# Kernel tuning notes

Hardware: AMD Instinct MI355X
Metric: run time of the kernel (lower is better)

Reference implementation:

```python
import math
import jax, jax.numpy as jnp
import numpy as np
from jax import lax

B = 32768
D = 1024          # input_dim
LAT = 64          # latent_dim
S_SLOTS = 32
L_SLOTS = 256


def setup_inputs() -> dict:
    key = jax.random.key(0)
    ks = jax.random.split(key, 8)
    inp = {
        "query": jax.random.normal(ks[0], (B, D), dtype=jnp.float32),
        "short_term_bank": jax.random.normal(ks[1], (S_SLOTS, D), dtype=jnp.float32) * 0.02,
        "long_term_bank": jax.random.normal(ks[2], (L_SLOTS, LAT), dtype=jnp.float32) * 0.02,
        # long_term_decoder: Linear(LAT -> D), stored as (in, out)
        "dec_w": jax.random.normal(ks[3], (LAT, D), dtype=jnp.float32) / math.sqrt(LAT),
        "dec_b": jnp.zeros((D,), dtype=jnp.float32),
        # query_proj: Linear(D -> LAT)
        "q_w": jax.random.normal(ks[4], (D, LAT), dtype=jnp.float32) / math.sqrt(D),
        "q_b": jnp.zeros((LAT,), dtype=jnp.float32),
        # short_query_proj: Linear(D -> D)
        "sq_w": jax.random.normal(ks[5], (D, D), dtype=jnp.float32) / math.sqrt(D),
        "sq_b": jnp.zeros((D,), dtype=jnp.float32),
        "top_k_short": 4,
        "top_k_long": 8,
    }
    return inp


def reference(query, short_term_bank, long_term_bank, dec_w, dec_b,
              q_w, q_b, sq_w, sq_b, top_k_short, top_k_long):
    # ---- short-term hierarchy ----
    short_query = query @ sq_w + sq_b                                   # (B, D)
    s_scores = jax.nn.softmax(
        (short_query @ short_term_bank.T) * (1.0 / math.sqrt(D)), axis=-1)  # (B, S_SLOTS)
    s_top, s_idx = lax.top_k(s_scores, top_k_short)                     # (B, k_s)
    s_gather = short_term_bank[s_idx]                                   # (B, k_s, D)
    short_retrieved = jnp.einsum('bk,bkd->bd', s_top, s_gather)         # (B, D)

    # ---- long-term hierarchy ----
    long_query = query @ q_w + q_b                                      # (B, LAT)
    l_scores = jax.nn.softmax(
        (long_query @ long_term_bank.T) * (1.0 / math.sqrt(LAT)), axis=-1)  # (B, L_SLOTS)
    l_top, l_idx = lax.top_k(l_scores, top_k_long)                      # (B, k_l)
    long_latent = long_term_bank[l_idx]                                 # (B, k_l, LAT)
    long_dec = long_latent @ dec_w + dec_b                              # (B, k_l, D)
    long_retrieved = jnp.einsum('bk,bkd->bd', l_top, long_dec)          # (B, D)

    retrieved = short_retrieved + long_retrieved                        # (B, D)
    return retrieved, s_idx, l_idx, s_top, l_top
```

## Files before the change

### kernel.cpp

```cpp
#include <hip/hip_runtime.h>
#include <math.h>

#define BROWS 32768
#define DIM   1024
#define NLAT  64
#define NS    32
#define NL    256
#define RPB   32


__global__ void prep_w2(const float* __restrict__ sq_w,
                        const float* __restrict__ sbank,
                        const float* __restrict__ sq_b,
                        double* __restrict__ W2d,
                        double* __restrict__ sconst)
{
    int t = blockIdx.x * blockDim.x + threadIdx.x;
    int s = t & (NS - 1);
    int d = t >> 5;
    const float* wr = sq_w + (size_t)d * DIM;
    const float* br = sbank + (size_t)s * DIM;
    double acc = 0.0;
    for (int o = 0; o < DIM; ++o) acc += (double)wr[o] * (double)br[o];
    W2d[(size_t)d * NS + s] = acc * 0.03125;
    if (d == 0) {
        double c = 0.0;
        for (int o = 0; o < DIM; ++o) c += (double)sq_b[o] * (double)br[o];
        sconst[s] = c * 0.03125;
    }
}


__device__ __forceinline__ void fma4(float4& A, float wgt, const float4& v) {
    A.x += wgt * v.x; A.y += wgt * v.y; A.z += wgt * v.z; A.w += wgt * v.w;
}

__device__ __forceinline__ float np_expf(float x) {
    float m = rintf(x * 1.44269504088896341f);
    float r = fmaf(m, -0.693359375f, x);
    r = fmaf(m, 2.12194440e-4f, r);
    float y = 1.9875691500E-4f;
    y = fmaf(y, r, 1.3981999507E-3f);
    y = fmaf(y, r, 8.3334519073E-3f);
    y = fmaf(y, r, 4.1665795894E-2f);
    y = fmaf(y, r, 1.6666665459E-1f);
    y = fmaf(y, r, 5.0000001201E-1f);
    float r2 = r * r;
    y = fmaf(y, r2, r);
    y = y + 1.0f;
    return ldexpf(y, (int)m);
}


__global__ __launch_bounds__(256, 4)
void hmb_main(const float* __restrict__ query,
              const float* __restrict__ qw,
              const float* __restrict__ qb,
              const double* __restrict__ W2d,
              const double* __restrict__ sconst,
              const float* __restrict__ lbank,
              const float* __restrict__ dec_w,
              const float* __restrict__ dec_b,
              const float* __restrict__ sbank,
              float* __restrict__ out)
{
    __shared__ __align__(16) unsigned char raw[34176];
    float  (*LqF)[64]  = (float  (*)[64])(raw);
    float  (*Sc)[256]  = (float  (*)[256])(raw + 8192);
    float  (*Wd)[256]  = (float  (*)[256])(raw);
    double (*Pl)[33]   = (double (*)[33])(raw + 16384);
    float  (*Zl)[64]   = (float  (*)[64])(raw + 24832);
    int    (*SWi)[4]   = (int    (*)[4])(raw + 33024);
    float  (*SWv)[4]   = (float  (*)[4])(raw + 33536);
    float  *SLT        = (float  *)(raw + 34048);

    const int t    = threadIdx.x;
    const int lane = t & 63;
    const int wv   = t >> 6;
    const int row0 = blockIdx.x * RPB;

    const size_t OS_SIDX = 33554432ull;
    const size_t OS_LIDX = 33685504ull;
    const size_t OS_STOP = 33947648ull;
    const size_t OS_LTOP = 34078720ull;

    {
        const float* qrow = query + (size_t)(row0 + 8 * wv) * DIM;
        const int  sIdx = lane & 31;
        const bool hi   = lane >= 32;
        float lt[8] = {0, 0, 0, 0, 0, 0, 0, 0};
        double av0 = 0, av1 = 0, av2 = 0, av3 = 0;
#pragma unroll 1
        for (int s = 0; s < 3; ++s) {
            const int dlo = s * 384;
            const int dhi = (s == 2) ? 1024 : (dlo + 384);
            float la[8] = {0, 0, 0, 0, 0, 0, 0, 0};
#pragma unroll 4
            for (int d = dlo; d < dhi; ++d) {
                float wl = qw[(size_t)d * NLAT + lane];
                float q0 = qrow[d];
                float q1 = qrow[DIM + d];
                float q2 = qrow[2 * DIM + d];
                float q3 = qrow[3 * DIM + d];
                float q4 = qrow[4 * DIM + d];
                float q5 = qrow[5 * DIM + d];
                float q6 = qrow[6 * DIM + d];
                float q7 = qrow[7 * DIM + d];
                la[0] = fmaf(q0, wl, la[0]);
                la[1] = fmaf(q1, wl, la[1]);
                la[2] = fmaf(q2, wl, la[2]);
                la[3] = fmaf(q3, wl, la[3]);
                la[4] = fmaf(q4, wl, la[4]);
                la[5] = fmaf(q5, wl, la[5]);
                la[6] = fmaf(q6, wl, la[6]);
                la[7] = fmaf(q7, wl, la[7]);
                double w2 = W2d[(size_t)d * NS + sIdx];
                av0 = fma((double)(hi ? q4 : q0), w2, av0);
                av1 = fma((double)(hi ? q5 : q1), w2, av1);
                av2 = fma((double)(hi ? q6 : q2), w2, av2);
                av3 = fma((double)(hi ? q7 : q3), w2, av3);
            }
#pragma unroll
            for (int i = 0; i < 8; ++i) lt[i] += la[i];
        }
        float qbl = qb[lane];
#pragma unroll
        for (int i = 0; i < 8; ++i)
            LqF[8 * wv + i][lane] = lt[i] + qbl;
        double sc = sconst[sIdx];
        int rbase = 8 * wv + (hi ? 4 : 0);
        Pl[sIdx][rbase + 0] = av0 + sc;
        Pl[sIdx][rbase + 1] = av1 + sc;
        Pl[sIdx][rbase + 2] = av2 + sc;
        Pl[sIdx][rbase + 3] = av3 + sc;
    }
    __syncthreads();

#pragma unroll 1
    for (int qtr = 0; qtr < 4; ++qtr) {
        {
            float acc[8];
#pragma unroll
            for (int rr = 0; rr < 8; ++rr) acc[rr] = 0.0f;
            const float4* lb4 = (const float4*)(lbank + (size_t)t * NLAT);
#pragma unroll 1
            for (int jq = 0; jq < 16; ++jq) {
                float4 b = lb4[jq];
#pragma unroll
                for (int rr = 0; rr < 8; ++rr) {
                    float4 q4v = *(const float4*)&LqF[8 * qtr + rr][4 * jq];
                    float a = acc[rr];
                    a = fmaf(q4v.x, b.x, a);
                    a = fmaf(q4v.y, b.y, a);
                    a = fmaf(q4v.z, b.z, a);
                    a = fmaf(q4v.w, b.w, a);
                    acc[rr] = a;
                }
            }
#pragma unroll
            for (int rr = 0; rr < 8; ++rr) Sc[rr][t] = acc[rr] * 0.125f;
        }
        __syncthreads();

#pragma unroll 1
        for (int rg = 0; rg < 2; ++rg) {
            const int rh  = 2 * wv + rg;
            const int row = 8 * qtr + rh;
            const size_t grow = (size_t)(row0 + row);
            float c0 = Sc[rh][lane],       c1 = Sc[rh][lane + 64],
                  c2 = Sc[rh][lane + 128], c3 = Sc[rh][lane + 192];
            float m = fmaxf(fmaxf(c0, c1), fmaxf(c2, c3));
#pragma unroll
            for (int off = 32; off > 0; off >>= 1)
                m = fmaxf(m, __shfl_xor(m, off, 64));
            float e0 = np_expf(c0 - m), e1 = np_expf(c1 - m),
                  e2 = np_expf(c2 - m), e3 = np_expf(c3 - m);
            float A0 = e0 + __shfl_down(e0, 16, 64);
            float B0 = __shfl_down(e0, 32, 64) + __shfl_down(e0, 48, 64);
            float C0 = e1 + __shfl_down(e1, 16, 64);
            float D0 = __shfl_down(e1, 32, 64) + __shfl_down(e1, 48, 64);
            float R0 = (A0 + B0) + (C0 + D0);
            float A1_ = e2 + __shfl_down(e2, 16, 64);
            float B1_ = __shfl_down(e2, 32, 64) + __shfl_down(e2, 48, 64);
            float C1_ = e3 + __shfl_down(e3, 16, 64);
            float D1_ = __shfl_down(e3, 32, 64) + __shfl_down(e3, 48, 64);
            float R1 = (A1_ + B1_) + (C1_ + D1_);
            float t0 = R0 + __shfl_down(R0, 8, 64);
            float u0 = t0 + __shfl_down(t0, 4, 64);
            float f0 = (u0 + __shfl_down(u0, 2, 64)) + (__shfl_down(u0, 1, 64) + __shfl_down(u0, 3, 64));
            float t1 = R1 + __shfl_down(R1, 8, 64);
            float u1 = t1 + __shfl_down(t1, 4, 64);
            float f1 = (u1 + __shfl_down(u1, 2, 64)) + (__shfl_down(u1, 1, 64) + __shfl_down(u1, 3, 64));
            float sden = __shfl(f0 + f1, 0, 64);
            float v0 = e0 / sden, v1 = e1 / sden, v2 = e2 / sden, v3 = e3 / sden;
            float ltv[8]; int lwi[8];
#pragma unroll
            for (int it = 0; it < 8; ++it) {
                float v = v0; int u = 0;
                if (v1 > v) { v = v1; u = 1; }
                if (v2 > v) { v = v2; u = 2; }
                if (v3 > v) { v = v3; u = 3; }
                int gi = lane + (u << 6);
#pragma unroll
                for (int off = 32; off > 0; off >>= 1) {
                    float ov = __shfl_xor(v, off, 64);
                    int og = __shfl_xor(gi, off, 64);
                    if (ov > v || (ov == v && og < gi)) { v = ov; gi = og; }
                }
                ltv[it] = v; lwi[it] = gi;
                if ((gi & 63) == lane) {
                    int wu = gi >> 6;
                    if      (wu == 0) v0 = -1.0e30f;
                    else if (wu == 1) v1 = -1.0e30f;
                    else if (wu == 2) v2 = -1.0e30f;
                    else              v3 = -1.0e30f;
                }
            }
            float zv = 0.0f;
#pragma unroll
            for (int k = 0; k < 8; ++k)
                zv += ltv[k] * lbank[(size_t)lwi[k] * NLAT + lane];
            Zl[row][lane] = zv;
            if (lane == 0) {
                SLT[row] = ltv[0]+ltv[1]+ltv[2]+ltv[3]+ltv[4]+ltv[5]+ltv[6]+ltv[7];
            } else if (lane == 1) {
                float* pi = out + OS_LIDX + grow * 8;
                float* pt = out + OS_LTOP + grow * 8;
#pragma unroll
                for (int k = 0; k < 8; ++k) { pi[k] = (float)lwi[k]; pt[k] = ltv[k]; }
            }
        }
        __syncthreads();
    }

#pragma unroll 1
    for (int rg = 0; rg < 8; ++rg) {
        const int r = 8 * wv + rg;
        const size_t grow = (size_t)(row0 + r);

        double sx0 = (lane < NS) ? Pl[lane][r] : -1.0e300;
        double sx = sx0;
        double swv_[4]; int swi_[4];
#pragma unroll
        for (int it = 0; it < 4; ++it) {
            double v = sx; int ix = lane;
#pragma unroll
            for (int off = 32; off > 0; off >>= 1) {
                double ov = __shfl_xor(v, off, 64);
                int oi = __shfl_xor(ix, off, 64);
                if (ov > v || (ov == v && oi < ix)) { v = ov; ix = oi; }
            }
            swv_[it] = v; swi_[it] = ix;
            if (lane == ix) sx = -1.0e300;
        }
        double sm = swv_[0];
        double ssum = (lane < NS) ? (double)expf((float)(sx0 - sm)) : 0.0;
#pragma unroll
        for (int off = 32; off > 0; off >>= 1) ssum += __shfl_xor(ssum, off, 64);
        float stv[4];
#pragma unroll
        for (int it = 0; it < 4; ++it)
            stv[it] = (float)((double)expf((float)(swv_[it] - sm)) / ssum);

        if (lane == 0) {
#pragma unroll
            for (int k = 0; k < 4; ++k) { SWi[r][k] = swi_[k]; SWv[r][k] = stv[k]; }
            float* ps = out + OS_SIDX + grow * 4;
            float* pt = out + OS_STOP + grow * 4;
#pragma unroll
            for (int k = 0; k < 4; ++k) { ps[k] = (float)swi_[k]; pt[k] = stv[k]; }
        }
    }

    const int rgrp = t >> 6;
    const int col4 = t & 63;

#pragma unroll 1
    for (int dc = 0; dc < 4; ++dc) {
        const int cbase = dc * 256 + 4 * col4;
        float4 db = *(const float4*)(dec_b + cbase);
        float4 acc3[8];
#pragma unroll
        for (int r8 = 0; r8 < 8; ++r8) {
            const int row = rgrp * 8 + r8;
            float slt = SLT[row];
            float4 a;
            a.x = slt * db.x; a.y = slt * db.y; a.z = slt * db.z; a.w = slt * db.w;
#pragma unroll
            for (int k = 0; k < 4; ++k) {
                int   si = SWi[row][k];
                float sv = SWv[row][k];
                float4 sb = *(const float4*)(sbank + (size_t)si * DIM + cbase);
                fma4(a, sv, sb);
            }
            acc3[r8] = a;
        }
#pragma unroll 1
        for (int jh = 0; jh < 4; ++jh) {
            __syncthreads();
#pragma unroll
            for (int i = 0; i < 4; ++i) {
                int e = t + 256 * i;
                int jr = e >> 6, c4 = e & 63;
                *(float4*)&Wd[jr][4 * c4] =
                    *(const float4*)(dec_w + (size_t)(16 * jh + jr) * DIM + dc * 256 + 4 * c4);
            }
            __syncthreads();
#pragma unroll 4
            for (int j2 = 0; j2 < 16; ++j2) {
                float4 w4 = *(const float4*)&Wd[j2][4 * col4];
#pragma unroll
                for (int r8 = 0; r8 < 8; ++r8) {
                    float z = Zl[rgrp * 8 + r8][16 * jh + j2];
                    fma4(acc3[r8], z, w4);
                }
            }
        }
#pragma unroll
        for (int r8 = 0; r8 < 8; ++r8) {
            const int row = rgrp * 8 + r8;
            *(float4*)(out + (size_t)(row0 + row) * DIM + cbase) = acc3[r8];
        }
    }
}


extern "C" void kernel_launch(void* const* d_in, const int* in_sizes, int n_in,
                              void* d_out, int out_size, void* d_ws, size_t ws_size,
                              hipStream_t stream) {
    const float* query = (const float*)d_in[0];
    const float* sbank = (const float*)d_in[1];
    const float* lbank = (const float*)d_in[2];
    const float* dec_w = (const float*)d_in[3];
    const float* dec_b = (const float*)d_in[4];
    const float* q_w   = (const float*)d_in[5];
    const float* q_b   = (const float*)d_in[6];
    const float* sq_w  = (const float*)d_in[7];
    const float* sq_b  = (const float*)d_in[8];
    float* out = (float*)d_out;

    char* ws = (char*)d_ws;
    double* W2d    = (double*)(ws);
    double* sconst = (double*)(ws + 262144);

    prep_w2 <<<dim3(128), dim3(256), 0, stream>>>(sq_w, sbank, sq_b, W2d, sconst);
    hmb_main<<<dim3(BROWS / RPB), dim3(256), 0, stream>>>(
        query, q_w, q_b, W2d, sconst, lbank, dec_w, dec_b, sbank, out);
}
```

Before: 662.3 us.

## Keep short-term scores in registers, vectorize loads, raise occupancy to five blocks

Removes the shared-memory Pl buffer and instead passes the double-precision short-term score accumulators through wave shuffles into the top-k stage. This shrinks LDS from about 34KB to about 25KB, and launch bounds are raised to 5 blocks per CU. The projection loop now uses float4 query loads, with per-lane query rows chosen by pointer instead of selects. The decoder inner loop reads Zl as float4 with four Wd rows at a time. The risks are that the registers held across phases (the double accumulators) together with the tighter launch bound may cause spills, and that the larger query load footprint may raise register pressure.

```diff
diff --git a/kernel.cpp b/kernel.cpp
--- a/kernel.cpp
+++ b/kernel.cpp
@@ -52,7 +52,7 @@
 }
 
 
-__global__ __launch_bounds__(256, 4)
+__global__ __launch_bounds__(256, 5)
 void hmb_main(const float* __restrict__ query,
               const float* __restrict__ qw,
               const float* __restrict__ qb,
@@ -64,15 +64,14 @@
               const float* __restrict__ sbank,
               float* __restrict__ out)
 {
-    __shared__ __align__(16) unsigned char raw[34176];
+    __shared__ __align__(16) unsigned char raw[25728];
     float  (*LqF)[64]  = (float  (*)[64])(raw);
     float  (*Sc)[256]  = (float  (*)[256])(raw + 8192);
     float  (*Wd)[256]  = (float  (*)[256])(raw);
-    double (*Pl)[33]   = (double (*)[33])(raw + 16384);
-    float  (*Zl)[64]   = (float  (*)[64])(raw + 24832);
-    int    (*SWi)[4]   = (int    (*)[4])(raw + 33024);
-    float  (*SWv)[4]   = (float  (*)[4])(raw + 33536);
-    float  *SLT        = (float  *)(raw + 34048);
+    float  (*Zl)[64]   = (float  (*)[64])(raw + 16384);
+    int    (*SWi)[4]   = (int    (*)[4])(raw + 24576);
+    float  (*SWv)[4]   = (float  (*)[4])(raw + 25088);
+    float  *SLT        = (float  *)(raw + 25600);
 
     const int t    = threadIdx.x;
     const int lane = t & 63;
@@ -84,41 +83,64 @@
     const size_t OS_STOP = 33947648ull;
     const size_t OS_LTOP = 34078720ull;
 
+    double av0 = 0, av1 = 0, av2 = 0, av3 = 0;
+    const int  sIdx = lane & 31;
+    const bool hi   = lane >= 32;
     {
         const float* qrow = query + (size_t)(row0 + 8 * wv) * DIM;
-        const int  sIdx = lane & 31;
-        const bool hi   = lane >= 32;
+        const float* qfp  = qrow + (hi ? 4 * (size_t)DIM : 0);
         float lt[8] = {0, 0, 0, 0, 0, 0, 0, 0};
-        double av0 = 0, av1 = 0, av2 = 0, av3 = 0;
 #pragma unroll 1
         for (int s = 0; s < 3; ++s) {
             const int dlo = s * 384;
             const int dhi = (s == 2) ? 1024 : (dlo + 384);
             float la[8] = {0, 0, 0, 0, 0, 0, 0, 0};
-#pragma unroll 4
-            for (int d = dlo; d < dhi; ++d) {
-                float wl = qw[(size_t)d * NLAT + lane];
-                float q0 = qrow[d];
-                float q1 = qrow[DIM + d];
-                float q2 = qrow[2 * DIM + d];
-                float q3 = qrow[3 * DIM + d];
-                float q4 = qrow[4 * DIM + d];
-                float q5 = qrow[5 * DIM + d];
-                float q6 = qrow[6 * DIM + d];
-                float q7 = qrow[7 * DIM + d];
-                la[0] = fmaf(q0, wl, la[0]);
-                la[1] = fmaf(q1, wl, la[1]);
-                la[2] = fmaf(q2, wl, la[2]);
-                la[3] = fmaf(q3, wl, la[3]);
-                la[4] = fmaf(q4, wl, la[4]);
-                la[5] = fmaf(q5, wl, la[5]);
-                la[6] = fmaf(q6, wl, la[6]);
-                la[7] = fmaf(q7, wl, la[7]);
-                double w2 = W2d[(size_t)d * NS + sIdx];
-                av0 = fma((double)(hi ? q4 : q0), w2, av0);
-                av1 = fma((double)(hi ? q5 : q1), w2, av1);
-                av2 = fma((double)(hi ? q6 : q2), w2, av2);
-                av3 = fma((double)(hi ? q7 : q3), w2, av3);
+#pragma unroll 1
+            for (int d = dlo; d < dhi; d += 4) {
+                float4 qv0 = *(const float4*)(qrow + d);
+                float4 qv1 = *(const float4*)(qrow + DIM + d);
+                float4 qv2 = *(const float4*)(qrow + 2 * DIM + d);
+                float4 qv3 = *(const float4*)(qrow + 3 * DIM + d);
+                float4 qv4 = *(const float4*)(qrow + 4 * DIM + d);
+                float4 qv5 = *(const float4*)(qrow + 5 * DIM + d);
+                float4 qv6 = *(const float4*)(qrow + 6 * DIM + d);
+                float4 qv7 = *(const float4*)(qrow + 7 * DIM + d);
+                float4 qs0 = *(const float4*)(qfp + d);
+                float4 qs1 = *(const float4*)(qfp + DIM + d);
+                float4 qs2 = *(const float4*)(qfp + 2 * DIM + d);
+                float4 qs3 = *(const float4*)(qfp + 3 * DIM + d);
+                float wl0 = qw[(size_t)(d)     * NLAT + lane];
+                float wl1 = qw[(size_t)(d + 1) * NLAT + lane];
+                float wl2 = qw[(size_t)(d + 2) * NLAT + lane];
+                float wl3 = qw[(size_t)(d + 3) * NLAT + lane];
+                double w20 = W2d[(size_t)(d)     * NS + sIdx];
+                double w21 = W2d[(size_t)(d + 1) * NS + sIdx];
+                double w22 = W2d[(size_t)(d + 2) * NS + sIdx];
+                double w23 = W2d[(size_t)(d + 3) * NS + sIdx];
+                la[0] = fmaf(qv0.x, wl0, la[0]); la[1] = fmaf(qv1.x, wl0, la[1]);
+                la[2] = fmaf(qv2.x, wl0, la[2]); la[3] = fmaf(qv3.x, wl0, la[3]);
+                la[4] = fmaf(qv4.x, wl0, la[4]); la[5] = fmaf(qv5.x, wl0, la[5]);
+                la[6] = fmaf(qv6.x, wl0, la[6]); la[7] = fmaf(qv7.x, wl0, la[7]);
+                av0 = fma((double)qs0.x, w20, av0); av1 = fma((double)qs1.x, w20, av1);
+                av2 = fma((double)qs2.x, w20, av2); av3 = fma((double)qs3.x, w20, av3);
+                la[0] = fmaf(qv0.y, wl1, la[0]); la[1] = fmaf(qv1.y, wl1, la[1]);
+                la[2] = fmaf(qv2.y, wl1, la[2]); la[3] = fmaf(qv3.y, wl1, la[3]);
+                la[4] = fmaf(qv4.y, wl1, la[4]); la[5] = fmaf(qv5.y, wl1, la[5]);
+                la[6] = fmaf(qv6.y, wl1, la[6]); la[7] = fmaf(qv7.y, wl1, la[7]);
+                av0 = fma((double)qs0.y, w21, av0); av1 = fma((double)qs1.y, w21, av1);
+                av2 = fma((double)qs2.y, w21, av2); av3 = fma((double)qs3.y, w21, av3);
+                la[0] = fmaf(qv0.z, wl2, la[0]); la[1] = fmaf(qv1.z, wl2, la[1]);
+                la[2] = fmaf(qv2.z, wl2, la[2]); la[3] = fmaf(qv3.z, wl2, la[3]);
+                la[4] = fmaf(qv4.z, wl2, la[4]); la[5] = fmaf(qv5.z, wl2, la[5]);
+                la[6] = fmaf(qv6.z, wl2, la[6]); la[7] = fmaf(qv7.z, wl2, la[7]);
+                av0 = fma((double)qs0.z, w22, av0); av1 = fma((double)qs1.z, w22, av1);
+                av2 = fma((double)qs2.z, w22, av2); av3 = fma((double)qs3.z, w22, av3);
+                la[0] = fmaf(qv0.w, wl3, la[0]); la[1] = fmaf(qv1.w, wl3, la[1]);
+                la[2] = fmaf(qv2.w, wl3, la[2]); la[3] = fmaf(qv3.w, wl3, la[3]);
+                la[4] = fmaf(qv4.w, wl3, la[4]); la[5] = fmaf(qv5.w, wl3, la[5]);
+                la[6] = fmaf(qv6.w, wl3, la[6]); la[7] = fmaf(qv7.w, wl3, la[7]);
+                av0 = fma((double)qs0.w, w23, av0); av1 = fma((double)qs1.w, w23, av1);
+                av2 = fma((double)qs2.w, w23, av2); av3 = fma((double)qs3.w, w23, av3);
             }
 #pragma unroll
             for (int i = 0; i < 8; ++i) lt[i] += la[i];
@@ -127,12 +149,6 @@
 #pragma unroll
         for (int i = 0; i < 8; ++i)
             LqF[8 * wv + i][lane] = lt[i] + qbl;
-        double sc = sconst[sIdx];
-        int rbase = 8 * wv + (hi ? 4 : 0);
-        Pl[sIdx][rbase + 0] = av0 + sc;
-        Pl[sIdx][rbase + 1] = av1 + sc;
-        Pl[sIdx][rbase + 2] = av2 + sc;
-        Pl[sIdx][rbase + 3] = av3 + sc;
     }
     __syncthreads();
 
@@ -233,42 +249,48 @@
         __syncthreads();
     }
 
-#pragma unroll 1
-    for (int rg = 0; rg < 8; ++rg) {
-        const int r = 8 * wv + rg;
-        const size_t grow = (size_t)(row0 + r);
-
-        double sx0 = (lane < NS) ? Pl[lane][r] : -1.0e300;
-        double sx = sx0;
-        double swv_[4]; int swi_[4];
-#pragma unroll
-        for (int it = 0; it < 4; ++it) {
-            double v = sx; int ix = lane;
-#pragma unroll
-            for (int off = 32; off > 0; off >>= 1) {
-                double ov = __shfl_xor(v, off, 64);
-                int oi = __shfl_xor(ix, off, 64);
-                if (ov > v || (ov == v && oi < ix)) { v = ov; ix = oi; }
-            }
-            swv_[it] = v; swi_[it] = ix;
-            if (lane == ix) sx = -1.0e300;
-        }
-        double sm = swv_[0];
-        double ssum = (lane < NS) ? (double)expf((float)(sx0 - sm)) : 0.0;
-#pragma unroll
-        for (int off = 32; off > 0; off >>= 1) ssum += __shfl_xor(ssum, off, 64);
-        float stv[4];
-#pragma unroll
-        for (int it = 0; it < 4; ++it)
-            stv[it] = (float)((double)expf((float)(swv_[it] - sm)) / ssum);
-
-        if (lane == 0) {
-#pragma unroll
-            for (int k = 0; k < 4; ++k) { SWi[r][k] = swi_[k]; SWv[r][k] = stv[k]; }
-            float* ps = out + OS_SIDX + grow * 4;
-            float* pt = out + OS_STOP + grow * 4;
-#pragma unroll
-            for (int k = 0; k < 4; ++k) { ps[k] = (float)swi_[k]; pt[k] = stv[k]; }
+    {
+        double scv = sconst[sIdx];
+#pragma unroll
+        for (int rg = 0; rg < 8; ++rg) {
+            const int r = 8 * wv + rg;
+            const size_t grow = (size_t)(row0 + r);
+            double avc = ((rg & 3) == 0) ? av0 : ((rg & 3) == 1) ? av1
+                       : ((rg & 3) == 2) ? av2 : av3;
+            int src = (lane & 31) + ((rg & 4) ? 32 : 0);
+            double pv = __shfl(avc, src, 64);
+            double sx0 = (lane < NS) ? (pv + scv) : -1.0e300;
+            double sx = sx0;
+            double swv_[4]; int swi_[4];
+#pragma unroll
+            for (int it = 0; it < 4; ++it) {
+                double v = sx; int ix = lane;
+#pragma unroll
+                for (int off = 32; off > 0; off >>= 1) {
+                    double ov = __shfl_xor(v, off, 64);
+                    int oi = __shfl_xor(ix, off, 64);
+                    if (ov > v || (ov == v && oi < ix)) { v = ov; ix = oi; }
+                }
+                swv_[it] = v; swi_[it] = ix;
+                if (lane == ix) sx = -1.0e300;
+            }
+            double sm = swv_[0];
+            double ssum = (lane < NS) ? (double)expf((float)(sx0 - sm)) : 0.0;
+#pragma unroll
+            for (int off = 32; off > 0; off >>= 1) ssum += __shfl_xor(ssum, off, 64);
+            float stv[4];
+#pragma unroll
+            for (int it = 0; it < 4; ++it)
+                stv[it] = (float)((double)expf((float)(swv_[it] - sm)) / ssum);
+
+            if (lane == 0) {
+#pragma unroll
+                for (int k = 0; k < 4; ++k) { SWi[r][k] = swi_[k]; SWv[r][k] = stv[k]; }
+                float* ps = out + OS_SIDX + grow * 4;
+                float* pt = out + OS_STOP + grow * 4;
+#pragma unroll
+                for (int k = 0; k < 4; ++k) { ps[k] = (float)swi_[k]; pt[k] = stv[k]; }
+            }
         }
     }
 
@@ -306,13 +328,19 @@
                     *(const float4*)(dec_w + (size_t)(16 * jh + jr) * DIM + dc * 256 + 4 * c4);
             }
             __syncthreads();
-#pragma unroll 4
-            for (int j2 = 0; j2 < 16; ++j2) {
-                float4 w4 = *(const float4*)&Wd[j2][4 * col4];
+#pragma unroll 1
+            for (int j2g = 0; j2g < 4; ++j2g) {
+                float4 w40 = *(const float4*)&Wd[4 * j2g + 0][4 * col4];
+                float4 w41 = *(const float4*)&Wd[4 * j2g + 1][4 * col4];
+                float4 w42 = *(const float4*)&Wd[4 * j2g + 2][4 * col4];
+                float4 w43 = *(const float4*)&Wd[4 * j2g + 3][4 * col4];
 #pragma unroll
                 for (int r8 = 0; r8 < 8; ++r8) {
-                    float z = Zl[rgrp * 8 + r8][16 * jh + j2];
-                    fma4(acc3[r8], z, w4);
+                    float4 zv = *(const float4*)&Zl[rgrp * 8 + r8][16 * jh + 4 * j2g];
+                    fma4(acc3[r8], zv.x, w40);
+                    fma4(acc3[r8], zv.y, w41);
+                    fma4(acc3[r8], zv.z, w42);
+                    fma4(acc3[r8], zv.w, w43);
                 }
             }
         }
```

Result: slower. 798.1 us (+20.5%).
